# Kernel optimization log

Hardware: AMD Instinct MI355X
Metric: run time of the kernel (lower is better)

The kernel has to match this reference:

```python
import jax, jax.numpy as jnp
import numpy as np

EMB = 1024
SHARED_MLP = 2048
MOE_MLP = 1024
N_EXPERTS = 8
TOP_K = 2
EPS = 1e-6


def rms_norm(x, scale=None, eps=EPS):
    # MaxText RMSNorm: x * rsqrt(mean(x^2)+eps) [* scale]
    y = x * jax.lax.rsqrt(jnp.mean(jnp.square(x), axis=-1, keepdims=True) + eps)
    return y if scale is None else y * scale


def setup_inputs() -> dict:
    key = jax.random.key(0)
    ks = jax.random.split(key, 12)
    B, S, D, F, M, E = 2, 2048, EMB, SHARED_MLP, MOE_MLP, N_EXPERTS
    sd = D ** -0.5
    sm = M ** -0.5
    sf = F ** -0.5
    return {
        "inputs": jax.random.normal(ks[0], (B, S, D), jnp.float32),
        "original_inputs": jax.random.normal(ks[1], (B, S, D), jnp.float32),
        # norm scales (init ~ ones with small perturbation for non-trivial math)
        "pre_forward_scale": 1.0 + 0.02 * jax.random.normal(ks[2], (D,), jnp.float32),
        "pre_ff_ln2_scale": 1.0 + 0.02 * jax.random.normal(ks[3], (D,), jnp.float32),
        "post_ff_ln1_scale": 1.0 + 0.02 * jax.random.normal(ks[4], (D,), jnp.float32),
        "post_ff_ln2_scale": 1.0 + 0.02 * jax.random.normal(ks[5], (D,), jnp.float32),
        # router and routed expert weights
        "router_w": jax.random.normal(ks[6], (D, E), jnp.float32) * sd,
        "e_wi0": jax.random.normal(ks[7], (E, D, M), jnp.float32) * sd,
        "e_wi1": jax.random.normal(ks[8], (E, D, M), jnp.float32) * sd,
        "e_wo": jax.random.normal(ks[9], (E, M, D), jnp.float32) * sm,
        # shared expert (gated MLP)
        "s_wi0": jax.random.normal(ks[10], (D, F), jnp.float32) * sd,
        "s_wi1": jax.random.normal(ks[11], (D, F), jnp.float32) * sd,
        "s_wo": jax.random.normal(jax.random.fold_in(key, 99), (F, D), jnp.float32) * sf,
    }


def _forward(inputs, original_inputs, pre_forward_scale, pre_ff_ln2_scale,
             post_ff_ln1_scale, post_ff_ln2_scale, router_w,
             e_wi0, e_wi1, e_wo, s_wi0, s_wi1, s_wo):
    B, S, D = inputs.shape
    E, K = N_EXPERTS, TOP_K
    # ---- shared experts: gated GeLU MLP on `inputs` ----
    h_sh = jax.nn.gelu(jnp.einsum('bsd,df->bsf', inputs, s_wi0)) * \
           jnp.einsum('bsd,df->bsf', inputs, s_wi1)
    shared = jnp.einsum('bsf,fd->bsd', h_sh, s_wo)
    shared = rms_norm(shared, post_ff_ln1_scale)
    # ---- gate-norm scaling (no-scale RMSNorm * emb^-0.5 * learned scale) ----
    routed_in = rms_norm(original_inputs, pre_ff_ln2_scale)
    gate_in = rms_norm(original_inputs) * (D ** -0.5) * pre_forward_scale  # f32 gate
    # ---- routing: softmax logits, top-k, renormalized combine weights ----
    logits = jnp.einsum('bsd,de->bse', gate_in.astype(jnp.float32), router_w)
    probs = jax.nn.softmax(logits, axis=-1)                       # [B,S,E]
    top_w, top_i = jax.lax.top_k(probs, K)                        # [B,S,K]
    top_w = top_w / jnp.sum(top_w, axis=-1, keepdims=True)
    onehot = jax.nn.one_hot(top_i, E, dtype=probs.dtype)          # [B,S,K,E]
    combine = jnp.einsum('bske,bsk->bse', onehot, top_w)          # [B,S,E]
    # ---- dropless routed experts: dense per-expert gated FFN + weighted combine ----
    x = routed_in.reshape(B * S, D)                               # [T,D]
    cw = combine.reshape(B * S, E)                                # [T,E]
    h = jax.nn.gelu(jnp.einsum('td,edm->etm', x, e_wi0)) * \
        jnp.einsum('td,edm->etm', x, e_wi1)                       # [E,T,M]
    routed = jnp.einsum('etm,emd,te->td', h, e_wo, cw)            # [T,D]
    routed = rms_norm(routed.reshape(B, S, D), post_ff_ln2_scale)
    # ---- load-balance aux loss (switch-style) ----
    frac_tokens = jnp.mean(jnp.sum(onehot, axis=-2), axis=(0, 1)) / K  # [E]
    frac_probs = jnp.mean(probs, axis=(0, 1))                          # [E]
    lb_loss = E * jnp.sum(frac_tokens * frac_probs)
    return routed + shared, lb_loss


def reference(inputs, original_inputs, pre_forward_scale, pre_ff_ln2_scale,
              post_ff_ln1_scale, post_ff_ln2_scale, router_w,
              e_wi0, e_wi1, e_wo, s_wi0, s_wi1, s_wo):
    out, lb_loss = _forward(inputs, original_inputs, pre_forward_scale,
                            pre_ff_ln2_scale, post_ff_ln1_scale, post_ff_ln2_scale,
                            router_w, e_wi0, e_wi1, e_wo, s_wi0, s_wi1, s_wo)
    return out, lb_loss
```

## Files before the change

### kernel.cpp

```cpp
#include <hip/hip_runtime.h>
#include <stdint.h>


typedef unsigned short u16;
typedef u16 u16x4 __attribute__((ext_vector_type(4)));
typedef u16 u16x8 __attribute__((ext_vector_type(8)));
typedef _Float16 f16x8 __attribute__((ext_vector_type(8)));
typedef float f32x4 __attribute__((ext_vector_type(4)));
typedef __attribute__((address_space(1))) void* as1_vp;
typedef __attribute__((address_space(3))) void* as3_vp;

#define T_TOK 4096
#define DIM   1024
#define FDIM  2048
#define MDIM  1024
#define NEXP  8
#define MAXTILES 72
#define HROWS (MAXTILES * 128)

__device__ __forceinline__ u16 f2h(float f) {
  _Float16 h = (_Float16)f;
  return __builtin_bit_cast(u16, h);
}
__device__ __forceinline__ float h2f(u16 u) {
  return (float)__builtin_bit_cast(_Float16, u);
}
__device__ __forceinline__ float gelu_f(float x) {
  const float y2 = x * (1.5957691216f + 0.0713548163f * x * x);
  return x / (1.0f + __expf(-y2));
}
__device__ __forceinline__ void async_copy16(const void* g, void* l) {
  __builtin_amdgcn_global_load_lds((as1_vp)(uintptr_t)g,
                                   (as3_vp)(uint32_t)(uintptr_t)l, 16, 0, 0);
}
__device__ __forceinline__ f16x8 lds_frag(const u16* p) {
  return __builtin_bit_cast(f16x8, *(const u16x8*)p);
}

__global__ __launch_bounds__(256, 2) void gemm_in(
    const u16* __restrict__ xs, const u16* __restrict__ swi_t,
    const u16* __restrict__ routed, const u16* __restrict__ ewi_t,
    u16* __restrict__ Hs, u16* __restrict__ Hr,
    const int* __restrict__ ridx, const int2* __restrict__ tdesc,
    const int* __restrict__ n_tiles) {
  const int yb = (int)blockIdx.y;
  const u16 *A, *B0t, *B1t;
  u16* H;
  int N;
  long bm;
  bool gather;
  if (yb < 32) {
    bm = (long)yb * 128;
    A = xs;
    B0t = swi_t;
    B1t = swi_t + (size_t)FDIM * DIM;
    H = Hs;
    N = FDIM;
    gather = false;
  } else {
    const int ty = yb - 32;
    if (ty >= *n_tiles) return;
    if ((int)blockIdx.x >= MDIM / 128) return;
    const int2 td = tdesc[ty];
    bm = td.y;
    A = routed;
    B0t = ewi_t + (long)td.x * MDIM * DIM;
    B1t = ewi_t + (size_t)NEXP * MDIM * DIM + (long)td.x * MDIM * DIM;
    H = Hr;
    N = MDIM;
    gather = true;
  }
  __shared__ __align__(16) u16 As[128 * 64];
  __shared__ __align__(16) u16 Bs0[128 * 64];
  __shared__ __align__(16) u16 Bs1[128 * 64];
  const int tid = threadIdx.x;
  const int lane = tid & 63;
  const int wave = tid >> 6;
  const int wm = (wave >> 1) * 64;
  const int wn = (wave & 1) * 64;
  const long bn = (long)blockIdx.x * 128;

  f32x4 acc0[4][4] = {}, acc1[4][4] = {};

  const int r0 = tid >> 3;
  const int cc = ((tid & 7) ^ (r0 & 7)) * 8;
  const long rowstride = 32 * (long)DIM;
  const u16* Ag[4];
  if (gather) {
#pragma unroll
    for (int i = 0; i < 4; i++) Ag[i] = A + (long)ridx[bm + r0 + i * 32] * DIM + cc;
  } else {
#pragma unroll
    for (int i = 0; i < 4; i++) Ag[i] = A + (bm + r0 + i * 32) * (long)DIM + cc;
  }
  const u16* B0g = B0t + (bn + r0) * (long)DIM + cc;
  const u16* B1g = B1t + (bn + r0) * (long)DIM + cc;
  const int fr = lane & 15;
  const int fq = lane >> 4;

  for (int k0 = 0; k0 < DIM; k0 += 64) {
#pragma unroll
    for (int i = 0; i < 4; i++) {
      async_copy16(Ag[i] + k0, &As[tid * 8 + i * 2048]);
      async_copy16(B0g + i * rowstride + k0, &Bs0[tid * 8 + i * 2048]);
      async_copy16(B1g + i * rowstride + k0, &Bs1[tid * 8 + i * 2048]);
    }
    __syncthreads();
#pragma unroll
    for (int kc = 0; kc < 8; kc += 4) {
      f16x8 af[4], b0[4], b1[4];
      const int q = (fq + kc) ^ (fr & 7);
#pragma unroll
      for (int i = 0; i < 4; i++) {
        af[i] = lds_frag(&As[(wm + i * 16 + fr) * 64 + q * 8]);
        b0[i] = lds_frag(&Bs0[(wn + i * 16 + fr) * 64 + q * 8]);
        b1[i] = lds_frag(&Bs1[(wn + i * 16 + fr) * 64 + q * 8]);
      }
#pragma unroll
      for (int mi = 0; mi < 4; mi++)
#pragma unroll
        for (int ni = 0; ni < 4; ni++) {
          acc0[mi][ni] = __builtin_amdgcn_mfma_f32_16x16x32_f16(af[mi], b0[ni], acc0[mi][ni], 0, 0, 0);
          acc1[mi][ni] = __builtin_amdgcn_mfma_f32_16x16x32_f16(af[mi], b1[ni], acc1[mi][ni], 0, 0, 0);
        }
    }
    __syncthreads();
  }

  const int er = (lane >> 4) * 4;
  const int ec = lane & 15;
#pragma unroll
  for (int mi = 0; mi < 4; mi++)
#pragma unroll
    for (int r = 0; r < 4; r++) {
      const long row = bm + wm + mi * 16 + er + r;
#pragma unroll
      for (int ni = 0; ni < 4; ni++)
        H[row * N + bn + wn + ni * 16 + ec] =
            f2h(gelu_f(acc0[mi][ni][r]) * acc1[mi][ni][r]);
    }
}

__global__ __launch_bounds__(256) void gemm_out2(
    const u16* __restrict__ Hs, const u16* __restrict__ swo_t,
    float* __restrict__ racc, const u16* __restrict__ Hr,
    const u16* __restrict__ ewo_t, float* __restrict__ Hout,
    const int2* __restrict__ tdesc, const int* __restrict__ n_tiles) {
  const int yb = (int)blockIdx.y;
  const u16 *A, *Bt;
  float* C;
  long bm;
  int Kfull, Khalf;
  if (yb < 32) {
    bm = (long)yb * 128;
    A = Hs;
    Bt = swo_t;
    Kfull = FDIM;
    Khalf = FDIM / 2;
    C = racc + (long)blockIdx.z * T_TOK * DIM;
  } else {
    const int ty = yb - 32;
    if (ty >= *n_tiles) return;
    const int2 td = tdesc[ty];
    bm = td.y;
    A = Hr;
    Bt = ewo_t + (long)td.x * DIM * MDIM;
    Kfull = MDIM;
    Khalf = MDIM / 2;
    C = Hout + (long)blockIdx.z * HROWS * DIM;
  }
  __shared__ __align__(16) u16 As[128 * 64];
  __shared__ __align__(16) u16 Bs[128 * 64];
  const int tid = threadIdx.x;
  const int lane = tid & 63;
  const int wave = tid >> 6;
  const int wm = (wave >> 1) * 64;
  const int wn = (wave & 1) * 64;
  const long bn = (long)blockIdx.x * 128;
  const int kbase = blockIdx.z * Khalf;

  f32x4 acc[4][4] = {};
  const int r0 = tid >> 3;
  const int cc = ((tid & 7) ^ (r0 & 7)) * 8;
  const long rowstride = 32 * (long)Kfull;
  const u16* Ag[4];
#pragma unroll
  for (int i = 0; i < 4; i++) Ag[i] = A + (bm + r0 + i * 32) * (long)Kfull + kbase + cc;
  const u16* Bg = Bt + (bn + r0) * (long)Kfull + kbase + cc;
  const int fr = lane & 15;
  const int fq = lane >> 4;

  for (int k0 = 0; k0 < Khalf; k0 += 64) {
#pragma unroll
    for (int i = 0; i < 4; i++) {
      async_copy16(Ag[i] + k0, &As[tid * 8 + i * 2048]);
      async_copy16(Bg + i * rowstride + k0, &Bs[tid * 8 + i * 2048]);
    }
    __syncthreads();
#pragma unroll
    for (int kc = 0; kc < 8; kc += 4) {
      f16x8 af[4], bq[4];
      const int q = (fq + kc) ^ (fr & 7);
#pragma unroll
      for (int i = 0; i < 4; i++) {
        af[i] = lds_frag(&As[(wm + i * 16 + fr) * 64 + q * 8]);
        bq[i] = lds_frag(&Bs[(wn + i * 16 + fr) * 64 + q * 8]);
      }
#pragma unroll
      for (int mi = 0; mi < 4; mi++)
#pragma unroll
        for (int ni = 0; ni < 4; ni++)
          acc[mi][ni] = __builtin_amdgcn_mfma_f32_16x16x32_f16(af[mi], bq[ni], acc[mi][ni], 0, 0, 0);
    }
    __syncthreads();
  }

  const int er = (lane >> 4) * 4;
  const int ec = lane & 15;
#pragma unroll
  for (int mi = 0; mi < 4; mi++)
#pragma unroll
    for (int r = 0; r < 4; r++) {
      const long row = bm + wm + mi * 16 + er + r;
#pragma unroll
      for (int ni = 0; ni < 4; ni++)
        C[row * DIM + bn + wn + ni * 16 + ec] = acc[mi][ni][r];
    }
}

__global__ __launch_bounds__(256) void transpose_cvt2(
    const float* __restrict__ s0, const float* __restrict__ s1,
    u16* __restrict__ dst, int R, int C, int zsplit) {
  __shared__ float tile[32][33];
  const int z = blockIdx.z;
  const float* src = (z < zsplit) ? s0 + (long)z * R * C
                                  : s1 + (long)(z - zsplit) * R * C;
  u16* d = dst + (long)z * R * C;
  const int c0 = blockIdx.x * 32, r0 = blockIdx.y * 32;
  const int tx = threadIdx.x & 31, ty = threadIdx.x >> 5;
#pragma unroll
  for (int i = 0; i < 32; i += 8) tile[ty + i][tx] = src[(long)(r0 + ty + i) * C + c0 + tx];
  __syncthreads();
#pragma unroll
  for (int i = 0; i < 32; i += 8) d[(long)(c0 + ty + i) * R + r0 + tx] = f2h(tile[tx][ty + i]);
}

__global__ __launch_bounds__(256) void router_kernel(
    const float* __restrict__ orig, const float* __restrict__ inputs,
    const float* __restrict__ pfs, const float* __restrict__ ln2s,
    const float* __restrict__ rw, u16* __restrict__ routed_in,
    u16* __restrict__ x_sh, int* __restrict__ eidx, float* __restrict__ ewt,
    float* __restrict__ probs_out) {
  const int t = blockIdx.x;
  const int tid = threadIdx.x;
  const int d = tid * 4;
  {
    const float4 xi = *(const float4*)(inputs + (long)t * DIM + d);
    u16x4 xo = {f2h(xi.x), f2h(xi.y), f2h(xi.z), f2h(xi.w)};
    *(u16x4*)(x_sh + (long)t * DIM + d) = xo;
  }
  const float4 v = *(const float4*)(orig + (long)t * DIM + d);
  float ss = v.x * v.x + v.y * v.y + v.z * v.z + v.w * v.w;
#pragma unroll
  for (int off = 32; off > 0; off >>= 1) ss += __shfl_down(ss, off);
  __shared__ float red[4];
  __shared__ float lred[4][8];
  if ((tid & 63) == 0) red[tid >> 6] = ss;
  __syncthreads();
  const float rs = rsqrtf((red[0] + red[1] + red[2] + red[3]) * (1.0f / DIM) + 1e-6f);

  const float4 l2 = *(const float4*)(ln2s + d);
  u16x4 ro = {f2h(v.x * rs * l2.x), f2h(v.y * rs * l2.y), f2h(v.z * rs * l2.z),
              f2h(v.w * rs * l2.w)};
  *(u16x4*)(routed_in + (long)t * DIM + d) = ro;

  const float4 pf = *(const float4*)(pfs + d);
  const float c = rs * 0.03125f;
  const float g0 = v.x * c * pf.x, g1 = v.y * c * pf.y;
  const float g2 = v.z * c * pf.z, g3 = v.w * c * pf.w;
  float lg[8];
#pragma unroll
  for (int e = 0; e < 8; e++)
    lg[e] = g0 * rw[(d + 0) * 8 + e] + g1 * rw[(d + 1) * 8 + e] +
            g2 * rw[(d + 2) * 8 + e] + g3 * rw[(d + 3) * 8 + e];
#pragma unroll
  for (int e = 0; e < 8; e++)
#pragma unroll
    for (int off = 32; off > 0; off >>= 1) lg[e] += __shfl_down(lg[e], off);
  if ((tid & 63) == 0)
#pragma unroll
    for (int e = 0; e < 8; e++) lred[tid >> 6][e] = lg[e];
  __syncthreads();
  if (tid == 0) {
    float lz[8], p[8];
    float mx = -1e30f;
#pragma unroll
    for (int e = 0; e < 8; e++) {
      lz[e] = lred[0][e] + lred[1][e] + lred[2][e] + lred[3][e];
      mx = fmaxf(mx, lz[e]);
    }
    float s = 0.0f;
#pragma unroll
    for (int e = 0; e < 8; e++) {
      p[e] = expf(lz[e] - mx);
      s += p[e];
    }
    const float invs = 1.0f / s;
#pragma unroll
    for (int e = 0; e < 8; e++) p[e] *= invs;
    int i1 = 0;
    for (int e = 1; e < 8; e++)
      if (p[e] > p[i1]) i1 = e;
    int i2 = (i1 == 0) ? 1 : 0;
    for (int e = 0; e < 8; e++)
      if (e != i1 && p[e] > p[i2]) i2 = e;
    const float wsum = p[i1] + p[i2];
    eidx[2 * t] = i1;
    eidx[2 * t + 1] = i2;
    ewt[2 * t] = p[i1] / wsum;
    ewt[2 * t + 1] = p[i2] / wsum;
    float* prow = probs_out + (long)t * 8;
    for (int e = 0; e < 8; e++) prow[e] = p[e];
  }
}

__global__ __launch_bounds__(256) void bucket_count(const int* __restrict__ eidx,
                                                    int* __restrict__ counts) {
  __shared__ int lcnt[8];
  const int tid = threadIdx.x;
  if (tid < 8) lcnt[tid] = 0;
  __syncthreads();
  const int t = blockIdx.x * 256 + tid;
  atomicAdd(&lcnt[eidx[2 * t]], 1);
  atomicAdd(&lcnt[eidx[2 * t + 1]], 1);
  __syncthreads();
  if (tid < 8) atomicAdd(&counts[tid], lcnt[tid]);
}

__global__ void setup_tiles(const int* __restrict__ counts, int* __restrict__ poffset,
                            int2* __restrict__ tdesc, int* __restrict__ n_tiles) {
  if (threadIdx.x == 0 && blockIdx.x == 0) {
    int cur = 0, nt = 0;
    for (int e = 0; e < NEXP; e++) {
      poffset[e] = cur;
      const int ntile = (counts[e] + 127) >> 7;
      for (int i = 0; i < ntile; i++) {
        int2 d;
        d.x = e;
        d.y = cur + i * 128;
        tdesc[nt++] = d;
      }
      cur += ntile * 128;
    }
    n_tiles[0] = nt;
  }
}

__global__ __launch_bounds__(256) void bucket_scatter(
    const int* __restrict__ eidx, const int* __restrict__ poffset,
    int* __restrict__ cursors, int* __restrict__ ridx, int* __restrict__ pos) {
  __shared__ int lcnt[8], base[8];
  const int tid = threadIdx.x;
  if (tid < 8) lcnt[tid] = 0;
  __syncthreads();
  const int t = blockIdx.x * 256 + tid;
  const int e0 = eidx[2 * t], e1 = eidx[2 * t + 1];
  const int r0 = atomicAdd(&lcnt[e0], 1);
  const int r1 = atomicAdd(&lcnt[e1], 1);
  __syncthreads();
  if (tid < 8) base[tid] = atomicAdd(&cursors[tid], lcnt[tid]);
  __syncthreads();
  const int p0 = poffset[e0] + base[e0] + r0;
  const int p1 = poffset[e1] + base[e1] + r1;
  ridx[p0] = t;
  ridx[p1] = t;
  pos[2 * t] = p0;
  pos[2 * t + 1] = p1;
}

__global__ __launch_bounds__(256) void lb_reduce(const float* __restrict__ probs,
                                                 const int* __restrict__ counts,
                                                 float* __restrict__ out) {
  const int tid = threadIdx.x;
  float psum[8] = {};
  for (int tt = 0; tt < 16; tt++) {
    const long t = (long)tid * 16 + tt;
    const float4* pp = (const float4*)(probs + t * 8);
    const float4 p0 = pp[0], p1 = pp[1];
    psum[0] += p0.x; psum[1] += p0.y; psum[2] += p0.z; psum[3] += p0.w;
    psum[4] += p1.x; psum[5] += p1.y; psum[6] += p1.z; psum[7] += p1.w;
  }
#pragma unroll
  for (int e = 0; e < 8; e++)
#pragma unroll
    for (int off = 32; off > 0; off >>= 1) psum[e] += __shfl_down(psum[e], off);
  __shared__ float sp[4][8];
  if ((tid & 63) == 0)
#pragma unroll
    for (int e = 0; e < 8; e++) sp[tid >> 6][e] = psum[e];
  __syncthreads();
  if (tid == 0) {
    float loss = 0.0f;
#pragma unroll
    for (int e = 0; e < 8; e++) {
      const float fp = (sp[0][e] + sp[1][e] + sp[2][e] + sp[3][e]) / 4096.0f;
      const float ft = (float)counts[e] / (4096.0f * 2.0f);
      loss += ft * fp;
    }
    out[0] = 8.0f * loss;
  }
}

__global__ __launch_bounds__(256) void final_norm(
    const float* __restrict__ racc, const float* __restrict__ Hout,
    const int* __restrict__ pos, const float* __restrict__ ewt,
    const float* __restrict__ post1, const float* __restrict__ post2,
    float* __restrict__ out) {
  const int t = blockIdx.x;
  const int tid = threadIdx.x;
  const int d = tid * 4;
  const long base = (long)t * DIM + d;
  const float4 a = *(const float4*)(racc + base);
  const float4 b = *(const float4*)(racc + base + (long)T_TOK * DIM);
  float4 vs;
  vs.x = a.x + b.x; vs.y = a.y + b.y; vs.z = a.z + b.z; vs.w = a.w + b.w;
  const float w0 = ewt[2 * t], w1 = ewt[2 * t + 1];
  const long p0 = pos[2 * t], p1 = pos[2 * t + 1];
  const long SK = (long)HROWS * DIM;
  const float4 a0 = *(const float4*)(Hout + p0 * DIM + d);
  const float4 a1 = *(const float4*)(Hout + SK + p0 * DIM + d);
  const float4 b0 = *(const float4*)(Hout + p1 * DIM + d);
  const float4 b1 = *(const float4*)(Hout + SK + p1 * DIM + d);
  float4 vr;
  vr.x = w0 * (a0.x + a1.x) + w1 * (b0.x + b1.x);
  vr.y = w0 * (a0.y + a1.y) + w1 * (b0.y + b1.y);
  vr.z = w0 * (a0.z + a1.z) + w1 * (b0.z + b1.z);
  vr.w = w0 * (a0.w + a1.w) + w1 * (b0.w + b1.w);
  float ss = vs.x * vs.x + vs.y * vs.y + vs.z * vs.z + vs.w * vs.w;
  float sr = vr.x * vr.x + vr.y * vr.y + vr.z * vr.z + vr.w * vr.w;
#pragma unroll
  for (int off = 32; off > 0; off >>= 1) {
    ss += __shfl_down(ss, off);
    sr += __shfl_down(sr, off);
  }
  __shared__ float reds[4], redr[4];
  if ((tid & 63) == 0) {
    reds[tid >> 6] = ss;
    redr[tid >> 6] = sr;
  }
  __syncthreads();
  const float rss = rsqrtf((reds[0] + reds[1] + reds[2] + reds[3]) * (1.0f / DIM) + 1e-6f);
  const float rsr = rsqrtf((redr[0] + redr[1] + redr[2] + redr[3]) * (1.0f / DIM) + 1e-6f);
  const float4 s1 = *(const float4*)(post1 + d);
  const float4 s2 = *(const float4*)(post2 + d);
  float4 o;
  o.x = vs.x * rss * s1.x + vr.x * rsr * s2.x;
  o.y = vs.y * rss * s1.y + vr.y * rsr * s2.y;
  o.z = vs.z * rss * s1.z + vr.z * rsr * s2.z;
  o.w = vs.w * rss * s1.w + vr.w * rsr * s2.w;
  *(float4*)(out + base) = o;
}

extern "C" void kernel_launch(void* const* d_in, const int* in_sizes, int n_in,
                              void* d_out, int out_size, void* d_ws, size_t ws_size,
                              hipStream_t stream) {
  (void)in_sizes; (void)n_in; (void)out_size; (void)ws_size;
  const float* inputs   = (const float*)d_in[0];
  const float* orig     = (const float*)d_in[1];
  const float* pfs      = (const float*)d_in[2];
  const float* ln2s     = (const float*)d_in[3];
  const float* post1    = (const float*)d_in[4];
  const float* post2    = (const float*)d_in[5];
  const float* router_w = (const float*)d_in[6];
  const float* e_wi0    = (const float*)d_in[7];
  const float* e_wi1    = (const float*)d_in[8];
  const float* e_wo     = (const float*)d_in[9];
  const float* s_wi0    = (const float*)d_in[10];
  const float* s_wi1    = (const float*)d_in[11];
  const float* s_wo     = (const float*)d_in[12];

  char* ws = (char*)d_ws;
  size_t o = 0;
  auto alloc = [&](size_t bytes) -> void* {
    void* p = ws + o;
    o += (bytes + 255) & ~(size_t)255;
    return p;
  };
  u16* s_wi_t  = (u16*)alloc((size_t)2 * FDIM * DIM * 2);
  u16* s_wo_t  = (u16*)alloc((size_t)DIM * FDIM * 2);
  u16* e_wi_t  = (u16*)alloc((size_t)2 * NEXP * MDIM * DIM * 2);
  u16* e_wo_t  = (u16*)alloc((size_t)NEXP * DIM * MDIM * 2);
  u16* x_sh    = (u16*)alloc((size_t)T_TOK * DIM * 2);
  u16* routed  = (u16*)alloc((size_t)T_TOK * DIM * 2);
  float* probs = (float*)alloc((size_t)T_TOK * 8 * 4);
  int* eidx    = (int*)alloc((size_t)T_TOK * 2 * 4);
  float* ewt   = (float*)alloc((size_t)T_TOK * 2 * 4);
  int* pos     = (int*)alloc((size_t)T_TOK * 2 * 4);
  int* imeta   = (int*)alloc(256);
  int* poffset = (int*)alloc(64);
  int* n_tiles = (int*)alloc(64);
  int2* tdesc  = (int2*)alloc(MAXTILES * 8);
  int* ridx    = (int*)alloc((size_t)HROWS * 4);
  float* racc  = (float*)alloc((size_t)2 * T_TOK * DIM * 4);
  u16* Hs      = (u16*)alloc((size_t)T_TOK * FDIM * 2);
  u16* H       = (u16*)alloc((size_t)HROWS * MDIM * 2);
  float* Hout  = (float*)alloc((size_t)2 * HROWS * DIM * 4);

  int* counts = imeta;
  int* cursors = imeta + 8;

  hipMemsetAsync(imeta, 0, 64, stream);
  hipMemsetAsync(ridx, 0, (size_t)HROWS * 4, stream);

  transpose_cvt2<<<dim3(FDIM / 32, DIM / 32, 2), 256, 0, stream>>>(
      s_wi0, s_wi1, s_wi_t, DIM, FDIM, 1);
  transpose_cvt2<<<dim3(DIM / 32, FDIM / 32, 1), 256, 0, stream>>>(
      s_wo, s_wo, s_wo_t, FDIM, DIM, 1);
  transpose_cvt2<<<dim3(MDIM / 32, DIM / 32, 16), 256, 0, stream>>>(
      e_wi0, e_wi1, e_wi_t, DIM, MDIM, 8);
  transpose_cvt2<<<dim3(DIM / 32, MDIM / 32, 8), 256, 0, stream>>>(
      e_wo, e_wo, e_wo_t, MDIM, DIM, 8);

  router_kernel<<<T_TOK, 256, 0, stream>>>(orig, inputs, pfs, ln2s, router_w,
                                           routed, x_sh, eidx, ewt, probs);

  bucket_count<<<16, 256, 0, stream>>>(eidx, counts);
  setup_tiles<<<1, 64, 0, stream>>>(counts, poffset, tdesc, n_tiles);
  bucket_scatter<<<16, 256, 0, stream>>>(eidx, poffset, cursors, ridx, pos);

  gemm_in<<<dim3(FDIM / 128, 32 + MAXTILES, 1), 256, 0, stream>>>(
      x_sh, s_wi_t, routed, e_wi_t, Hs, H, ridx, tdesc, n_tiles);

  gemm_out2<<<dim3(DIM / 128, 32 + MAXTILES, 2), 256, 0, stream>>>(
      Hs, s_wo_t, racc, H, e_wo_t, Hout, tdesc, n_tiles);

  final_norm<<<T_TOK, 256, 0, stream>>>(racc, Hout, pos, ewt, post1, post2,
                                        (float*)d_out);

  lb_reduce<<<1, 256, 0, stream>>>(probs, counts, (float*)d_out + (size_t)T_TOK * DIM);
}
```

Baseline: 441.2 us.

## Double-buffer GEMM LDS tiles with async prefetch and widen blocks to 128x256

Both grouped GEMM kernels move from a single-buffered 64-wide K tile with full barriers to a two-stage LDS ping-pong over 32-wide K slices. The prefetch of slice t+2 is issued while the MFMAs run on slice t, with explicit vmcnt/lgkmcnt waits and s_setprio around the MFMA block. Blocks grow to 512 threads covering 128x256 output tiles, so each A tile is reused across more N. The aim is to hide global-load latency and cut the number of barrier stalls, at the cost of fewer blocks per grid. gemm_in now needs about 80KB of LDS and a large register budget at 512 threads, which may limit occupancy.

```diff
diff --git a/kernel.cpp b/kernel.cpp
--- a/kernel.cpp
+++ b/kernel.cpp
@@ -37,7 +37,7 @@
   return __builtin_bit_cast(f16x8, *(const u16x8*)p);
 }
 
-__global__ __launch_bounds__(256, 2) void gemm_in(
+__global__ __launch_bounds__(512, 2) void gemm_in(
     const u16* __restrict__ xs, const u16* __restrict__ swi_t,
     const u16* __restrict__ routed, const u16* __restrict__ ewi_t,
     u16* __restrict__ Hs, u16* __restrict__ Hr,
@@ -60,7 +60,7 @@
   } else {
     const int ty = yb - 32;
     if (ty >= *n_tiles) return;
-    if ((int)blockIdx.x >= MDIM / 128) return;
+    if ((int)blockIdx.x >= MDIM / 256) return;
     const int2 td = tdesc[ty];
     bm = td.y;
     A = routed;
@@ -70,62 +70,74 @@
     N = MDIM;
     gather = true;
   }
-  __shared__ __align__(16) u16 As[128 * 64];
-  __shared__ __align__(16) u16 Bs0[128 * 64];
-  __shared__ __align__(16) u16 Bs1[128 * 64];
+  __shared__ __align__(16) u16 As[2][128 * 32];
+  __shared__ __align__(16) u16 Bs0[2][256 * 32];
+  __shared__ __align__(16) u16 Bs1[2][256 * 32];
   const int tid = threadIdx.x;
   const int lane = tid & 63;
   const int wave = tid >> 6;
-  const int wm = (wave >> 1) * 64;
-  const int wn = (wave & 1) * 64;
-  const long bn = (long)blockIdx.x * 128;
+  const int wm = (wave >> 2) * 64;
+  const int wn = (wave & 3) * 64;
+  const long bn = (long)blockIdx.x * 256;
 
   f32x4 acc0[4][4] = {}, acc1[4][4] = {};
 
-  const int r0 = tid >> 3;
-  const int cc = ((tid & 7) ^ (r0 & 7)) * 8;
-  const long rowstride = 32 * (long)DIM;
-  const u16* Ag[4];
-  if (gather) {
-#pragma unroll
-    for (int i = 0; i < 4; i++) Ag[i] = A + (long)ridx[bm + r0 + i * 32] * DIM + cc;
-  } else {
-#pragma unroll
-    for (int i = 0; i < 4; i++) Ag[i] = A + (bm + r0 + i * 32) * (long)DIM + cc;
-  }
-  const u16* B0g = B0t + (bn + r0) * (long)DIM + cc;
-  const u16* B1g = B1t + (bn + r0) * (long)DIM + cc;
+  const int r0 = tid >> 2;
+  const int cs = ((tid & 3) ^ ((r0 >> 1) & 3)) * 8;
+  const u16* Asrc = (gather ? A + (long)ridx[bm + r0] * DIM
+                            : A + (bm + r0) * (long)DIM) + cs;
+  const u16* B0a = B0t + (bn + r0) * (long)DIM + cs;
+  const u16* B0b = B0t + (bn + r0 + 128) * (long)DIM + cs;
+  const u16* B1a = B1t + (bn + r0) * (long)DIM + cs;
+  const u16* B1b = B1t + (bn + r0 + 128) * (long)DIM + cs;
   const int fr = lane & 15;
   const int fq = lane >> 4;
-
-  for (int k0 = 0; k0 < DIM; k0 += 64) {
+  const int qs = (fq ^ ((fr >> 1) & 3)) * 8;
+
+#define STAGE_IN(buf, kt)                                  \
+  {                                                        \
+    const int k0_ = (kt) * 32;                             \
+    async_copy16(Asrc + k0_, &As[buf][tid * 8]);           \
+    async_copy16(B0a + k0_, &Bs0[buf][tid * 8]);           \
+    async_copy16(B0b + k0_, &Bs0[buf][(tid + 512) * 8]);   \
+    async_copy16(B1a + k0_, &Bs1[buf][tid * 8]);           \
+    async_copy16(B1b + k0_, &Bs1[buf][(tid + 512) * 8]);   \
+  }
+
+  const int NT = DIM / 32;
+  STAGE_IN(0, 0);
+  STAGE_IN(1, 1);
+  int cur = 0;
+  for (int t = 0; t < NT; ++t) {
+    if (t + 2 < NT) {
+      asm volatile("s_waitcnt vmcnt(5)" ::: "memory");
+    } else {
+      asm volatile("s_waitcnt vmcnt(0)" ::: "memory");
+    }
+    __builtin_amdgcn_s_barrier();
+    f16x8 af[4], b0f[4], b1f[4];
 #pragma unroll
     for (int i = 0; i < 4; i++) {
-      async_copy16(Ag[i] + k0, &As[tid * 8 + i * 2048]);
-      async_copy16(B0g + i * rowstride + k0, &Bs0[tid * 8 + i * 2048]);
-      async_copy16(B1g + i * rowstride + k0, &Bs1[tid * 8 + i * 2048]);
-    }
-    __syncthreads();
-#pragma unroll
-    for (int kc = 0; kc < 8; kc += 4) {
-      f16x8 af[4], b0[4], b1[4];
-      const int q = (fq + kc) ^ (fr & 7);
-#pragma unroll
-      for (int i = 0; i < 4; i++) {
-        af[i] = lds_frag(&As[(wm + i * 16 + fr) * 64 + q * 8]);
-        b0[i] = lds_frag(&Bs0[(wn + i * 16 + fr) * 64 + q * 8]);
-        b1[i] = lds_frag(&Bs1[(wn + i * 16 + fr) * 64 + q * 8]);
+      af[i] = lds_frag(&As[cur][(wm + i * 16 + fr) * 32 + qs]);
+      b0f[i] = lds_frag(&Bs0[cur][(wn + i * 16 + fr) * 32 + qs]);
+      b1f[i] = lds_frag(&Bs1[cur][(wn + i * 16 + fr) * 32 + qs]);
+    }
+    asm volatile("s_waitcnt lgkmcnt(0)" ::: "memory");
+    __builtin_amdgcn_s_barrier();
+    asm volatile("" ::: "memory");
+    if (t + 2 < NT) STAGE_IN(cur, t + 2);
+    __builtin_amdgcn_s_setprio(1);
+#pragma unroll
+    for (int mi = 0; mi < 4; mi++)
+#pragma unroll
+      for (int ni = 0; ni < 4; ni++) {
+        acc0[mi][ni] = __builtin_amdgcn_mfma_f32_16x16x32_f16(af[mi], b0f[ni], acc0[mi][ni], 0, 0, 0);
+        acc1[mi][ni] = __builtin_amdgcn_mfma_f32_16x16x32_f16(af[mi], b1f[ni], acc1[mi][ni], 0, 0, 0);
       }
-#pragma unroll
-      for (int mi = 0; mi < 4; mi++)
-#pragma unroll
-        for (int ni = 0; ni < 4; ni++) {
-          acc0[mi][ni] = __builtin_amdgcn_mfma_f32_16x16x32_f16(af[mi], b0[ni], acc0[mi][ni], 0, 0, 0);
-          acc1[mi][ni] = __builtin_amdgcn_mfma_f32_16x16x32_f16(af[mi], b1[ni], acc1[mi][ni], 0, 0, 0);
-        }
-    }
-    __syncthreads();
-  }
+    __builtin_amdgcn_s_setprio(0);
+    cur ^= 1;
+  }
+#undef STAGE_IN
 
   const int er = (lane >> 4) * 4;
   const int ec = lane & 15;
@@ -141,7 +153,7 @@
     }
 }
 
-__global__ __launch_bounds__(256) void gemm_out2(
+__global__ __launch_bounds__(512, 2) void gemm_out2(
     const u16* __restrict__ Hs, const u16* __restrict__ swo_t,
     float* __restrict__ racc, const u16* __restrict__ Hr,
     const u16* __restrict__ ewo_t, float* __restrict__ Hout,
@@ -169,51 +181,65 @@
     Khalf = MDIM / 2;
     C = Hout + (long)blockIdx.z * HROWS * DIM;
   }
-  __shared__ __align__(16) u16 As[128 * 64];
-  __shared__ __align__(16) u16 Bs[128 * 64];
+  __shared__ __align__(16) u16 As[2][128 * 32];
+  __shared__ __align__(16) u16 Bs[2][256 * 32];
   const int tid = threadIdx.x;
   const int lane = tid & 63;
   const int wave = tid >> 6;
-  const int wm = (wave >> 1) * 64;
-  const int wn = (wave & 1) * 64;
-  const long bn = (long)blockIdx.x * 128;
+  const int wm = (wave >> 2) * 64;
+  const int wn = (wave & 3) * 64;
+  const long bn = (long)blockIdx.x * 256;
   const int kbase = blockIdx.z * Khalf;
 
   f32x4 acc[4][4] = {};
-  const int r0 = tid >> 3;
-  const int cc = ((tid & 7) ^ (r0 & 7)) * 8;
-  const long rowstride = 32 * (long)Kfull;
-  const u16* Ag[4];
-#pragma unroll
-  for (int i = 0; i < 4; i++) Ag[i] = A + (bm + r0 + i * 32) * (long)Kfull + kbase + cc;
-  const u16* Bg = Bt + (bn + r0) * (long)Kfull + kbase + cc;
+  const int r0 = tid >> 2;
+  const int cs = ((tid & 3) ^ ((r0 >> 1) & 3)) * 8;
+  const u16* Asrc = A + (bm + r0) * (long)Kfull + kbase + cs;
+  const u16* Ba = Bt + (bn + r0) * (long)Kfull + kbase + cs;
+  const u16* Bb = Bt + (bn + r0 + 128) * (long)Kfull + kbase + cs;
   const int fr = lane & 15;
   const int fq = lane >> 4;
-
-  for (int k0 = 0; k0 < Khalf; k0 += 64) {
+  const int qs = (fq ^ ((fr >> 1) & 3)) * 8;
+
+#define STAGE_OUT(buf, kt)                                \
+  {                                                       \
+    const int k0_ = (kt) * 32;                            \
+    async_copy16(Asrc + k0_, &As[buf][tid * 8]);          \
+    async_copy16(Ba + k0_, &Bs[buf][tid * 8]);            \
+    async_copy16(Bb + k0_, &Bs[buf][(tid + 512) * 8]);    \
+  }
+
+  const int NT = Khalf / 32;
+  STAGE_OUT(0, 0);
+  STAGE_OUT(1, 1);
+  int cur = 0;
+  for (int t = 0; t < NT; ++t) {
+    if (t + 2 < NT) {
+      asm volatile("s_waitcnt vmcnt(3)" ::: "memory");
+    } else {
+      asm volatile("s_waitcnt vmcnt(0)" ::: "memory");
+    }
+    __builtin_amdgcn_s_barrier();
+    f16x8 af[4], bf[4];
 #pragma unroll
     for (int i = 0; i < 4; i++) {
-      async_copy16(Ag[i] + k0, &As[tid * 8 + i * 2048]);
-      async_copy16(Bg + i * rowstride + k0, &Bs[tid * 8 + i * 2048]);
-    }
-    __syncthreads();
-#pragma unroll
-    for (int kc = 0; kc < 8; kc += 4) {
-      f16x8 af[4], bq[4];
-      const int q = (fq + kc) ^ (fr & 7);
-#pragma unroll
-      for (int i = 0; i < 4; i++) {
-        af[i] = lds_frag(&As[(wm + i * 16 + fr) * 64 + q * 8]);
-        bq[i] = lds_frag(&Bs[(wn + i * 16 + fr) * 64 + q * 8]);
-      }
-#pragma unroll
-      for (int mi = 0; mi < 4; mi++)
-#pragma unroll
-        for (int ni = 0; ni < 4; ni++)
-          acc[mi][ni] = __builtin_amdgcn_mfma_f32_16x16x32_f16(af[mi], bq[ni], acc[mi][ni], 0, 0, 0);
-    }
-    __syncthreads();
-  }
+      af[i] = lds_frag(&As[cur][(wm + i * 16 + fr) * 32 + qs]);
+      bf[i] = lds_frag(&Bs[cur][(wn + i * 16 + fr) * 32 + qs]);
+    }
+    asm volatile("s_waitcnt lgkmcnt(0)" ::: "memory");
+    __builtin_amdgcn_s_barrier();
+    asm volatile("" ::: "memory");
+    if (t + 2 < NT) STAGE_OUT(cur, t + 2);
+    __builtin_amdgcn_s_setprio(1);
+#pragma unroll
+    for (int mi = 0; mi < 4; mi++)
+#pragma unroll
+      for (int ni = 0; ni < 4; ni++)
+        acc[mi][ni] = __builtin_amdgcn_mfma_f32_16x16x32_f16(af[mi], bf[ni], acc[mi][ni], 0, 0, 0);
+    __builtin_amdgcn_s_setprio(0);
+    cur ^= 1;
+  }
+#undef STAGE_OUT
 
   const int er = (lane >> 4) * 4;
   const int ec = lane & 15;
@@ -528,10 +554,10 @@
   setup_tiles<<<1, 64, 0, stream>>>(counts, poffset, tdesc, n_tiles);
   bucket_scatter<<<16, 256, 0, stream>>>(eidx, poffset, cursors, ridx, pos);
 
-  gemm_in<<<dim3(FDIM / 128, 32 + MAXTILES, 1), 256, 0, stream>>>(
+  gemm_in<<<dim3(FDIM / 256, 32 + MAXTILES, 1), 512, 0, stream>>>(
       x_sh, s_wi_t, routed, e_wi_t, Hs, H, ridx, tdesc, n_tiles);
 
-  gemm_out2<<<dim3(DIM / 128, 32 + MAXTILES, 2), 256, 0, stream>>>(
+  gemm_out2<<<dim3(DIM / 256, 32 + MAXTILES, 2), 512, 0, stream>>>(
       Hs, s_wo_t, racc, H, e_wo_t, Hout, tdesc, n_tiles);
 
   final_norm<<<T_TOK, 256, 0, stream>>>(racc, Hout, pos, ewt, post1, post2,
```

Result: slower. 465.7 us (+5.6%).

## Remove split-K from output GEMM and drop partial-sum reduction

Applied to the files above, without the earlier changes.

The output projection GEMM no longer splits the K dimension across two z-slices. Each block now accumulates the full K range and writes a single fp32 result, so the partial buffers halve and final_norm reads one slice instead of summing two. This cuts global write/read traffic for partials, at the cost of half as many blocks and longer per-block loops, which may reduce latency hiding and load balance.

```diff
diff --git a/kernel.cpp b/kernel.cpp
--- a/kernel.cpp
+++ b/kernel.cpp
@@ -150,14 +150,13 @@
   const u16 *A, *Bt;
   float* C;
   long bm;
-  int Kfull, Khalf;
+  int K;
   if (yb < 32) {
     bm = (long)yb * 128;
     A = Hs;
     Bt = swo_t;
-    Kfull = FDIM;
-    Khalf = FDIM / 2;
-    C = racc + (long)blockIdx.z * T_TOK * DIM;
+    K = FDIM;
+    C = racc;
   } else {
     const int ty = yb - 32;
     if (ty >= *n_tiles) return;
@@ -165,9 +164,8 @@
     bm = td.y;
     A = Hr;
     Bt = ewo_t + (long)td.x * DIM * MDIM;
-    Kfull = MDIM;
-    Khalf = MDIM / 2;
-    C = Hout + (long)blockIdx.z * HROWS * DIM;
+    K = MDIM;
+    C = Hout;
   }
   __shared__ __align__(16) u16 As[128 * 64];
   __shared__ __align__(16) u16 Bs[128 * 64];
@@ -177,20 +175,19 @@
   const int wm = (wave >> 1) * 64;
   const int wn = (wave & 1) * 64;
   const long bn = (long)blockIdx.x * 128;
-  const int kbase = blockIdx.z * Khalf;
 
   f32x4 acc[4][4] = {};
   const int r0 = tid >> 3;
   const int cc = ((tid & 7) ^ (r0 & 7)) * 8;
-  const long rowstride = 32 * (long)Kfull;
+  const long rowstride = 32 * (long)K;
   const u16* Ag[4];
 #pragma unroll
-  for (int i = 0; i < 4; i++) Ag[i] = A + (bm + r0 + i * 32) * (long)Kfull + kbase + cc;
-  const u16* Bg = Bt + (bn + r0) * (long)Kfull + kbase + cc;
+  for (int i = 0; i < 4; i++) Ag[i] = A + (bm + r0 + i * 32) * (long)K + cc;
+  const u16* Bg = Bt + (bn + r0) * (long)K + cc;
   const int fr = lane & 15;
   const int fq = lane >> 4;
 
-  for (int k0 = 0; k0 < Khalf; k0 += 64) {
+  for (int k0 = 0; k0 < K; k0 += 64) {
 #pragma unroll
     for (int i = 0; i < 4; i++) {
       async_copy16(Ag[i] + k0, &As[tid * 8 + i * 2048]);
@@ -420,22 +417,16 @@
   const int tid = threadIdx.x;
   const int d = tid * 4;
   const long base = (long)t * DIM + d;
-  const float4 a = *(const float4*)(racc + base);
-  const float4 b = *(const float4*)(racc + base + (long)T_TOK * DIM);
-  float4 vs;
-  vs.x = a.x + b.x; vs.y = a.y + b.y; vs.z = a.z + b.z; vs.w = a.w + b.w;
+  const float4 vs = *(const float4*)(racc + base);
   const float w0 = ewt[2 * t], w1 = ewt[2 * t + 1];
   const long p0 = pos[2 * t], p1 = pos[2 * t + 1];
-  const long SK = (long)HROWS * DIM;
   const float4 a0 = *(const float4*)(Hout + p0 * DIM + d);
-  const float4 a1 = *(const float4*)(Hout + SK + p0 * DIM + d);
   const float4 b0 = *(const float4*)(Hout + p1 * DIM + d);
-  const float4 b1 = *(const float4*)(Hout + SK + p1 * DIM + d);
   float4 vr;
-  vr.x = w0 * (a0.x + a1.x) + w1 * (b0.x + b1.x);
-  vr.y = w0 * (a0.y + a1.y) + w1 * (b0.y + b1.y);
-  vr.z = w0 * (a0.z + a1.z) + w1 * (b0.z + b1.z);
-  vr.w = w0 * (a0.w + a1.w) + w1 * (b0.w + b1.w);
+  vr.x = w0 * a0.x + w1 * b0.x;
+  vr.y = w0 * a0.y + w1 * b0.y;
+  vr.z = w0 * a0.z + w1 * b0.z;
+  vr.w = w0 * a0.w + w1 * b0.w;
   float ss = vs.x * vs.x + vs.y * vs.y + vs.z * vs.z + vs.w * vs.w;
   float sr = vr.x * vr.x + vr.y * vr.y + vr.z * vr.z + vr.w * vr.w;
 #pragma unroll
@@ -501,10 +492,10 @@
   int* n_tiles = (int*)alloc(64);
   int2* tdesc  = (int2*)alloc(MAXTILES * 8);
   int* ridx    = (int*)alloc((size_t)HROWS * 4);
-  float* racc  = (float*)alloc((size_t)2 * T_TOK * DIM * 4);
+  float* racc  = (float*)alloc((size_t)T_TOK * DIM * 4);
   u16* Hs      = (u16*)alloc((size_t)T_TOK * FDIM * 2);
   u16* H       = (u16*)alloc((size_t)HROWS * MDIM * 2);
-  float* Hout  = (float*)alloc((size_t)2 * HROWS * DIM * 4);
+  float* Hout  = (float*)alloc((size_t)HROWS * DIM * 4);
 
   int* counts = imeta;
   int* cursors = imeta + 8;
@@ -531,7 +522,7 @@
   gemm_in<<<dim3(FDIM / 128, 32 + MAXTILES, 1), 256, 0, stream>>>(
       x_sh, s_wi_t, routed, e_wi_t, Hs, H, ridx, tdesc, n_tiles);
 
-  gemm_out2<<<dim3(DIM / 128, 32 + MAXTILES, 2), 256, 0, stream>>>(
+  gemm_out2<<<dim3(DIM / 128, 32 + MAXTILES, 1), 256, 0, stream>>>(
       Hs, s_wo_t, racc, H, e_wo_t, Hout, tdesc, n_tiles);
 
   final_norm<<<T_TOK, 256, 0, stream>>>(racc, Hout, pos, ewt, post1, post2,
```

Result: faster. 431.9 us (-2.1%).
